# Kernel optimization log

Hardware: AMD Instinct MI355X
Metric: run time of the kernel (lower is better)

## Reference

```python
import jax, jax.numpy as jnp
import numpy as np

Q, C, D, H, K, B, T = 10000, 200, 64, 64, 4, 512, 200
MAX_DISC = 10.0


def setup_inputs() -> dict:
    key = jax.random.key(0)
    ks = jax.random.split(key, 24)

    def p(k, shape, s=0.05):
        return jax.random.normal(k, shape, jnp.float32) * s

    mid_qd = (D + C) // 2   # 132
    mid_la = (H + C) // 2   # 132
    mid_dc = (D + 1) // 2   # 32
    inp = {
        'E_q': p(ks[0], (Q + 1, D)),
        'E_c': p(ks[1], (C + 1, D)),
        'E_it': p(ks[2], (101, D)),
        'E_ut': p(ks[3], (101, D)),
        'E_nh': p(ks[4], (101, D)),
        'W_fuse': p(ks[5], (D, 3 * D)), 'b_fuse': jnp.zeros((D,), jnp.float32),
        'W_ih': p(ks[6], (3 * H, 5 * D)), 'b_ih': jnp.zeros((3 * H,), jnp.float32),
        'W_hh': p(ks[7], (3 * H, H)), 'b_hh': jnp.zeros((3 * H,), jnp.float32),
        'qd_W1': p(ks[8], (mid_qd, D)), 'qd_b1': jnp.zeros((mid_qd,), jnp.float32),
        'qd_W2': p(ks[9], (C, mid_qd)), 'qd_b2': jnp.zeros((C,), jnp.float32),
        'la_W1': p(ks[10], (mid_la, H)), 'la_b1': jnp.zeros((mid_la,), jnp.float32),
        'la_W2': p(ks[11], (C, mid_la)), 'la_b2': jnp.zeros((C,), jnp.float32),
        'dc_W1': p(ks[12], (mid_dc, D)), 'dc_b1': jnp.zeros((mid_dc,), jnp.float32),
        'dc_W2': p(ks[13], (1, mid_dc)), 'dc_b2': jnp.zeros((1,), jnp.float32),
    }
    inp['question_seq'] = jax.random.randint(ks[14], (B, T), 0, Q + 1, jnp.int32)
    inp['correct_seq'] = jax.random.randint(ks[15], (B, T), 0, 2, jnp.int32)
    inp['interval_time_seq'] = jax.random.randint(ks[16], (B, T), 0, 101, jnp.int32)
    inp['use_time_seq'] = jax.random.randint(ks[17], (B, T), 0, 101, jnp.int32)
    inp['num_hint_seq'] = jax.random.randint(ks[18], (B, T), 0, 101, jnp.int32)
    inp['num_attempt_seq'] = jax.random.randint(ks[19], (B, T), 0, 101, jnp.int32)
    # per-question concept lists + padding mask (first nc entries valid)
    q2c = jax.random.randint(ks[20], (Q + 1, K), 0, C, jnp.int32)
    nc = jax.random.randint(ks[21], (Q + 1,), 1, K + 1, jnp.int32)
    mask = (jnp.arange(K, dtype=jnp.int32)[None, :] < nc[:, None]).astype(jnp.int32)
    inp['q2c_table'] = q2c
    inp['q2c_mask'] = mask
    rows = jnp.arange(Q + 1)[:, None]
    inp['Q_table'] = jnp.zeros((Q + 1, C), jnp.float32).at[rows, q2c].max(mask.astype(jnp.float32))
    return inp


def mlp2(x, W1, b1, W2, b2):
    # MLP4Proj, num_layer=2, eval-mode dropout == identity
    return jax.nn.relu(x @ W1.T + b1) @ W2.T + b2


def gru(x, W_ih, b_ih, W_hh, b_hh):
    # torch nn.GRU, 1 layer, batch_first; gate order r,z,n
    xp = jnp.einsum('btd,gd->btg', x, W_ih) + b_ih  # [B,T,3H]

    def step(h, xp_t):
        gh = h @ W_hh.T + b_hh
        xr, xz, xn = jnp.split(xp_t, 3, axis=-1)
        hr, hz, hn = jnp.split(gh, 3, axis=-1)
        r = jax.nn.sigmoid(xr + hr)
        z = jax.nn.sigmoid(xz + hz)
        n = jnp.tanh(xn + r * hn)
        h_new = (1.0 - z) * n + z * h
        return h_new, h_new

    h0 = jnp.zeros((x.shape[0], W_hh.shape[1]), x.dtype)
    _, hs = jax.lax.scan(step, h0, jnp.swapaxes(xp, 0, 1))
    return jnp.swapaxes(hs, 0, 1)  # [B,T,H]


def reference(E_q, E_c, E_it, E_ut, E_nh, W_fuse, b_fuse, W_ih, b_ih, W_hh, b_hh,
              qd_W1, qd_b1, qd_W2, qd_b2, la_W1, la_b1, la_W2, la_b2,
              dc_W1, dc_b1, dc_W2, dc_b2, Q_table,
              question_seq, correct_seq, interval_time_seq, use_time_seq,
              num_hint_seq, num_attempt_seq, q2c_table, q2c_mask):
    qe = E_q[question_seq]                                   # [B,T,D]
    # get_concept_emb: difficulty-weighted concept fusion
    qd = jax.nn.sigmoid(mlp2(qe, qd_W1, qd_b1, qd_W2, qd_b2))  # [B,T,C]
    qc_idx = q2c_table[question_seq]                          # [B,T,K]
    msk = q2c_mask[question_seq].astype(qe.dtype)             # [B,T,K]
    rel = jnp.take_along_axis(qd, qc_idx, axis=2) * msk       # [B,T,K]
    srel = rel.sum(-1, keepdims=True) + 1e-6
    ce = (rel[..., None] * E_c[qc_idx]).sum(-2) / srel        # [B,T,D]
    corr = jnp.broadcast_to(correct_seq[..., None].astype(qe.dtype), qe.shape)
    inter = jnp.concatenate([qe, ce, corr], axis=-1)          # [B,T,3D]
    # aux-info fusion (source bug: num_attempt also uses embed_num_hint)
    ut_nh_na = jnp.concatenate([E_ut[use_time_seq], E_nh[num_hint_seq], E_nh[num_attempt_seq]], axis=-1)
    fuse = ut_nh_na @ W_fuse.T + b_fuse                       # [B,T,D]
    x = jnp.concatenate([inter, E_it[interval_time_seq], fuse], axis=-1)  # [B,T,5D]
    latent = gru(x, W_ih, b_ih, W_hh, b_hh)                   # [B,T,H]
    # predict_score on shifted slices
    lat, qe2, qs2 = latent[:, :-1], qe[:, 1:], question_seq[:, 1:]
    ua = jax.nn.sigmoid(mlp2(lat, la_W1, la_b1, la_W2, la_b2))       # [B,T-1,C]
    disc = jax.nn.sigmoid(mlp2(qe2, dc_W1, dc_b1, dc_W2, dc_b2)) * MAX_DISC  # [B,T-1,1]
    qd2 = jax.nn.sigmoid(mlp2(qe2, qd_W1, qd_b1, qd_W2, qd_b2))      # [B,T-1,C]
    Qt = Q_table[qs2]                                                # [B,T-1,C]
    ua_m = ua * Qt
    qd_m = qd2 * Qt
    sw = qd_m.sum(-1, keepdims=True) + 1e-6
    y = disc * (ua_m - qd_m) / sw
    return jax.nn.sigmoid(y.sum(-1))                                 # [B,T-1]
```

## Files before the change

kernel.cpp:

```cpp
#include <hip/hip_runtime.h>
#include <hip/hip_fp16.h>

constexpr int QN  = 10001;
constexpr int BB  = 512;
constexpr int TT  = 200;
constexpr int QPB = 32;

__device__ __forceinline__ float sigm(float x) { return 1.f / (1.f + __expf(-x)); }
__device__ __forceinline__ float tanh_fast(float x) { return 1.f - 2.f / (1.f + __expf(2.f * x)); }

__device__ __forceinline__ unsigned packh_rtne(float lo, float hi) {
    return ((unsigned)__half_as_ushort(__float2half(hi)) << 16) |
            (unsigned)__half_as_ushort(__float2half(lo));
}

typedef _Float16 half2_t __attribute__((ext_vector_type(2)));
typedef float f4v __attribute__((ext_vector_type(4)));
__device__ __forceinline__ half2_t u2h(unsigned u) {
    union { unsigned u; half2_t h; } x; x.u = u; return x.h;
}

#if __has_builtin(__builtin_amdgcn_fdot2)
__device__ __forceinline__ float fdot2u(unsigned wu, unsigned hu, float acc) {
    return __builtin_amdgcn_fdot2(u2h(wu), u2h(hu), acc, false);
}
#else
__device__ __forceinline__ float fdot2u(unsigned wu, unsigned hu, float acc) {
    float wlo = __half2float(__ushort_as_half((unsigned short)(wu & 0xffffu)));
    float whi = __half2float(__ushort_as_half((unsigned short)(wu >> 16)));
    float hlo = __half2float(__ushort_as_half((unsigned short)(hu & 0xffffu)));
    float hhi = __half2float(__ushort_as_half((unsigned short)(hu >> 16)));
    return acc + wlo * hlo + whi * hhi;
}
#endif

typedef const __attribute__((address_space(1))) void cgv_t;
typedef __attribute__((address_space(3))) void lv_t;
__device__ __forceinline__ void glds16(const float* g, float* l) {
    __builtin_amdgcn_global_load_lds((cgv_t*)g, (lv_t*)l, 16, 0, 0);
}

__global__ void k_tables(const float* __restrict__ E_c, const float* __restrict__ E_it,
                         const float* __restrict__ E_ut, const float* __restrict__ E_nh,
                         const float* __restrict__ W_fuse, const float* __restrict__ b_fuse,
                         const float* __restrict__ W_ih, const float* __restrict__ b_ih,
                         const float* __restrict__ la_W1, const float* __restrict__ la_W2,
                         float* __restrict__ T_c, float* __restrict__ T_it,
                         float* __restrict__ T_ut, float* __restrict__ T_nh, float* __restrict__ T_na,
                         float* __restrict__ bias0, float* __restrict__ Vcorr,
                         unsigned* __restrict__ w1h, unsigned* __restrict__ w2h)
{
    int blk = blockIdx.x, j = threadIdx.x;
    __shared__ float s_e[64];
    __shared__ float s_t[64];
    const int ilv4 = (j & 63) * 4 + (j >> 6);

    if (blk < 201) {
        if (j < 64) s_e[j] = E_c[blk * 64 + j];
        __syncthreads();
        float a = 0.f;
        #pragma unroll
        for (int k = 0; k < 64; k++) a += W_ih[j * 320 + 64 + k] * s_e[k];
        T_c[blk * 192 + j] = a;
    } else if (blk < 302) {
        int r = blk - 201;
        if (j < 64) s_e[j] = E_it[r * 64 + j];
        __syncthreads();
        float a = 0.f;
        #pragma unroll
        for (int k = 0; k < 64; k++) a += W_ih[j * 320 + 192 + k] * s_e[k];
        T_it[r * 256 + ilv4] = a;
    } else if (blk < 605) {
        int which = (blk - 302) / 101;
        int r     = (blk - 302) % 101;
        const float* E = (which == 0) ? E_ut : E_nh;
        int fofs = which * 64;
        if (j < 64) s_e[j] = E[r * 64 + j];
        __syncthreads();
        if (j < 64) {
            float a = 0.f;
            #pragma unroll
            for (int d = 0; d < 64; d++) a += W_fuse[j * 192 + fofs + d] * s_e[d];
            s_t[j] = a;
        }
        __syncthreads();
        float a = 0.f;
        #pragma unroll
        for (int e = 0; e < 64; e++) a += W_ih[j * 320 + 256 + e] * s_t[e];
        float* outp = (which == 0) ? T_ut : ((which == 1) ? T_nh : T_na);
        outp[r * 256 + ilv4] = a;
    } else if (blk == 605) {
        float a = b_ih[j];
        #pragma unroll
        for (int e = 0; e < 64; e++) a += W_ih[j * 320 + 256 + e] * b_fuse[e];
        bias0[j] = a;
        float v = 0.f;
        #pragma unroll
        for (int k = 0; k < 64; k++) v += W_ih[j * 320 + 128 + k];
        Vcorr[j] = v;
    } else if (blk < 628) {
        int i = (blk - 606) * 192 + j;
        int m = i >> 5, k = i & 31;
        w1h[i] = packh_rtne(la_W1[m * 64 + 2 * k], la_W1[m * 64 + 2 * k + 1]);
    } else {
        int i = (blk - 628) * 192 + j;
        if (i < 200 * 68) {
            int c = i / 68, k = i - c * 68;
            w2h[i] = (k < 66) ? packh_rtne(la_W2[c * 132 + 2 * k], la_W2[c * 132 + 2 * k + 1]) : 0u;
        }
    }
}

__global__ void __launch_bounds__(192) k_perq(
    const float* __restrict__ E_q, const float* __restrict__ W_ih,
    const float* __restrict__ qd_W1, const float* __restrict__ qd_b1,
    const float* __restrict__ qd_W2, const float* __restrict__ qd_b2,
    const float* __restrict__ dc_W1, const float* __restrict__ dc_b1,
    const float* __restrict__ dc_W2, const float* __restrict__ dc_b2,
    const int* __restrict__ q2c, const int* __restrict__ q2cm,
    const float* __restrict__ T_c,
    float* __restrict__ Xq, float* __restrict__ disc,
    float* __restrict__ qds, float* __restrict__ wdk)
{
    __shared__ float s_wbuf[192 * 66];
    __shared__ float s_qe[QPB][64];
    __shared__ float s_wq[QPB][4];
    __shared__ int   s_cq[QPB][4];
    __shared__ float s_hidw[3][136];

    const int tid = threadIdx.x, w = tid >> 6, l = tid & 63;
    const int q0 = blockIdx.x * QPB;

    for (int i = tid; i < 132 * 64; i += 192)
        s_wbuf[(i >> 6) * 66 + (i & 63)] = qd_W1[i];
    for (int i = tid; i < 32 * 64; i += 192)
        s_wbuf[(132 + (i >> 6)) * 66 + (i & 63)] = dc_W1[i];
    for (int i = tid; i < QPB * 64; i += 192) {
        int qq = i >> 6, q = q0 + qq;
        s_qe[qq][i & 63] = E_q[(q < QN ? q : 0) * 64 + (i & 63)];
    }
    __syncthreads();

    for (int qq = w; qq < QPB; qq += 3) {
        int q = q0 + qq;
        bool valid = q < QN;
        int qc = valid ? q : 0;
        int cc[4], mm[4];
        #pragma unroll
        for (int k = 0; k < 4; k++) { cc[k] = q2c[qc * 4 + k]; mm[k] = q2cm[qc * 4 + k]; }

        float qe[64];
        #pragma unroll
        for (int k4 = 0; k4 < 16; k4++) {
            float4 v = *(const float4*)(&s_qe[qq][k4 * 4]);
            qe[4 * k4] = v.x; qe[4 * k4 + 1] = v.y; qe[4 * k4 + 2] = v.z; qe[4 * k4 + 3] = v.w;
        }

        auto rowdot = [&](int r) {
            const float* wr = s_wbuf + r * 66;
            float a0 = 0.f, a1 = 0.f, a2 = 0.f, a3 = 0.f;
            #pragma unroll
            for (int jj = 0; jj < 32; jj += 4) {
                float2 w0 = *(const float2*)(wr + 2 * jj);
                float2 w1 = *(const float2*)(wr + 2 * jj + 2);
                float2 w2 = *(const float2*)(wr + 2 * jj + 4);
                float2 w3 = *(const float2*)(wr + 2 * jj + 6);
                a0 += w0.x * qe[2 * jj]     + w0.y * qe[2 * jj + 1];
                a1 += w1.x * qe[2 * jj + 2] + w1.y * qe[2 * jj + 3];
                a2 += w2.x * qe[2 * jj + 4] + w2.y * qe[2 * jj + 5];
                a3 += w3.x * qe[2 * jj + 6] + w3.y * qe[2 * jj + 7];
            }
            return (a0 + a1) + (a2 + a3);
        };

        s_hidw[w][l]      = fmaxf(rowdot(l)      + qd_b1[l],      0.f);
        s_hidw[w][64 + l] = fmaxf(rowdot(64 + l) + qd_b1[64 + l], 0.f);
        if (l < 4)
            s_hidw[w][128 + l] = fmaxf(rowdot(128 + l) + qd_b1[128 + l], 0.f);
        float dch = 0.f;
        if (l < 32) dch = fmaxf(rowdot(132 + l) + dc_b1[l], 0.f);

        int g = l >> 4, li = l & 15;
        int c = cc[g];
        float acc = 0.f;
        #pragma unroll
        for (int i = 0; i < 9; i++) {
            int m = li + 16 * i;
            if (m < 132) acc += qd_W2[c * 132 + m] * s_hidw[w][m];
        }
        acc += __shfl_xor(acc, 1); acc += __shfl_xor(acc, 2);
        acc += __shfl_xor(acc, 4); acc += __shfl_xor(acc, 8);
        float r0 = __shfl(acc, 0), r1 = __shfl(acc, 16);
        float r2 = __shfl(acc, 32), r3 = __shfl(acc, 48);

        float raw[4] = { sigm(r0 + qd_b2[cc[0]]), sigm(r1 + qd_b2[cc[1]]),
                         sigm(r2 + qd_b2[cc[2]]), sigm(r3 + qd_b2[cc[3]]) };
        float rel[4];
        #pragma unroll
        for (int k = 0; k < 4; k++) rel[k] = raw[k] * (float)mm[k];
        float sr = rel[0] + rel[1] + rel[2] + rel[3] + 1e-6f;

        float qsum = 0.f, wdv[4];
        #pragma unroll
        for (int k = 0; k < 4; k++) {
            float wd = 0.f;
            if (mm[k]) {
                bool dup = false;
                for (int jj = 0; jj < k; jj++)
                    if (mm[jj] && cc[jj] == cc[k]) dup = true;
                if (!dup) { wd = 1.f; qsum += raw[k]; }
            }
            wdv[k] = wd;
        }
        if (l < 4) { s_wq[qq][l] = rel[l] / sr; s_cq[qq][l] = cc[l]; }
        if (valid) {
            if (l < 4) wdk[q * 4 + l] = wdv[l];
            if (l == 0) qds[q] = qsum;
        }

        float dv = (l < 32) ? dch * dc_W2[l] : 0.f;
        dv += __shfl_xor(dv, 1);  dv += __shfl_xor(dv, 2);
        dv += __shfl_xor(dv, 4);  dv += __shfl_xor(dv, 8);
        dv += __shfl_xor(dv, 16);
        if (valid && l == 0) disc[q] = sigm(dv + dc_b2[0]) * 10.f;
    }

    __syncthreads();
    for (int i = tid; i < 192 * 64; i += 192) {
        int r = i >> 6, k = i & 63;
        s_wbuf[r * 66 + k] = W_ih[r * 320 + k];
    }
    __syncthreads();

    for (int qq = w; qq < QPB; qq += 3) {
        int q = q0 + qq;
        if (q >= QN) continue;

        float qe[64];
        #pragma unroll
        for (int k4 = 0; k4 < 16; k4++) {
            float4 v = *(const float4*)(&s_qe[qq][k4 * 4]);
            qe[4 * k4] = v.x; qe[4 * k4 + 1] = v.y; qe[4 * k4 + 2] = v.z; qe[4 * k4 + 3] = v.w;
        }
        float wq[4]; int cq[4];
        #pragma unroll
        for (int k = 0; k < 4; k++) { wq[k] = s_wq[qq][k]; cq[k] = s_cq[qq][k]; }

        #pragma unroll
        for (int rr = 0; rr < 3; rr++) {
            int row = rr * 64 + l;
            const float* wr = s_wbuf + row * 66;
            float a0 = 0.f, a1 = 0.f, a2 = 0.f, a3 = 0.f;
            #pragma unroll
            for (int jj = 0; jj < 32; jj += 4) {
                float2 w0 = *(const float2*)(wr + 2 * jj);
                float2 w1 = *(const float2*)(wr + 2 * jj + 2);
                float2 w2 = *(const float2*)(wr + 2 * jj + 4);
                float2 w3 = *(const float2*)(wr + 2 * jj + 6);
                a0 += w0.x * qe[2 * jj]     + w0.y * qe[2 * jj + 1];
                a1 += w1.x * qe[2 * jj + 2] + w1.y * qe[2 * jj + 3];
                a2 += w2.x * qe[2 * jj + 4] + w2.y * qe[2 * jj + 5];
                a3 += w3.x * qe[2 * jj + 6] + w3.y * qe[2 * jj + 7];
            }
            float a = (a0 + a1) + (a2 + a3);
            #pragma unroll
            for (int k = 0; k < 4; k++) a += wq[k] * T_c[cq[k] * 192 + row];
            Xq[q * 256 + l * 4 + rr] = a;
        }
    }
}

__global__ void
__launch_bounds__(256)
__attribute__((amdgpu_waves_per_eu(1, 2)))
k_gru(
    const float* __restrict__ W_hh, const float* __restrict__ b_hh,
    const float* __restrict__ XqI, const float* __restrict__ TitI, const float* __restrict__ TutI,
    const float* __restrict__ TnhI, const float* __restrict__ TnaI,
    const float* __restrict__ b0, const float* __restrict__ vc,
    const int* __restrict__ qseq, const int* __restrict__ cseq, const int* __restrict__ itseq,
    const int* __restrict__ utseq, const int* __restrict__ nhseq, const int* __restrict__ naseq,
    const unsigned* __restrict__ w1h, const float* __restrict__ la_b1,
    const unsigned* __restrict__ w2h, const float* __restrict__ la_b2,
    const int* __restrict__ q2c,
    const float* __restrict__ disc, const float* __restrict__ qds,
    const float* __restrict__ wdk, float* __restrict__ out)
{
    const int tid = threadIdx.x, b = blockIdx.x;
    const int wave = tid >> 6, j = tid & 63;
    const int j4 = 4 * j;

    __shared__ float s_gb[4][5][64][4];
    __shared__ int s_ix[6 * TT];
    __shared__ unsigned s_hp[32];
    __shared__ float s_lat[TT][66];

    const int base = b * TT;
    for (int i = tid; i < TT; i += 256) {
        s_ix[i]          = qseq[base + i];
        s_ix[TT + i]     = cseq[base + i];
        s_ix[2 * TT + i] = itseq[base + i];
        s_ix[3 * TT + i] = utseq[base + i];
        s_ix[4 * TT + i] = nhseq[base + i];
        s_ix[5 * TT + i] = naseq[base + i];
    }
    if (tid < 32) s_hp[tid] = 0u;
    __syncthreads();

    if (wave == 0) {
        unsigned wr[32], wz[32], wn[32];
        {
            const float4* p0 = (const float4*)(W_hh + j * 64);
            const float4* p1 = (const float4*)(W_hh + (64 + j) * 64);
            const float4* p2 = (const float4*)(W_hh + (128 + j) * 64);
            #pragma unroll
            for (int k = 0; k < 16; k++) {
                float4 a = p0[k], bq = p1[k], c = p2[k];
                wr[2 * k] = packh_rtne(a.x, a.y);  wr[2 * k + 1] = packh_rtne(a.z, a.w);
                wz[2 * k] = packh_rtne(bq.x, bq.y); wz[2 * k + 1] = packh_rtne(bq.z, bq.w);
                wn[2 * k] = packh_rtne(c.x, c.y);  wn[2 * k + 1] = packh_rtne(c.z, c.w);
            }
        }
        #pragma unroll
        for (int k = 0; k < 32; k++)
            asm volatile("" : "+v"(wr[k]), "+v"(wz[k]), "+v"(wn[k]));

        const float bhr = b_hh[j], bhz = b_hh[64 + j], bhn = b_hh[128 + j];
        const float b0r = b0[j],   b0z = b0[64 + j],   b0n = b0[128 + j];
        const float vcr = vc[j],   vcz = vc[64 + j],   vcn = vc[128 + j];

        float hj = 0.f;
        float cA, cB, cC, cD;

#define GISSUE(S, CCV, tt) { \
        int q_ = s_ix[tt], c_ = s_ix[TT + tt], it_ = s_ix[2 * TT + tt]; \
        int ut_ = s_ix[3 * TT + tt], nh_ = s_ix[4 * TT + tt], na_ = s_ix[5 * TT + tt]; \
        CCV = (float)c_; \
        glds16(XqI  + q_  * 256 + j4, &s_gb[S][0][0][0]); \
        glds16(TitI + it_ * 256 + j4, &s_gb[S][1][0][0]); \
        glds16(TutI + ut_ * 256 + j4, &s_gb[S][2][0][0]); \
        glds16(TnhI + nh_ * 256 + j4, &s_gb[S][3][0][0]); \
        glds16(TnaI + na_ * 256 + j4, &s_gb[S][4][0][0]); \
    }

#define STEP(S, CCV, tcur, WN, REF) { \
        asm volatile("s_waitcnt vmcnt(" WN ")" ::: "memory"); \
        f4v g0 = *(const f4v*)&s_gb[S][0][j][0]; \
        f4v g1 = *(const f4v*)&s_gb[S][1][j][0]; \
        f4v g2 = *(const f4v*)&s_gb[S][2][j][0]; \
        f4v g3 = *(const f4v*)&s_gb[S][3][j][0]; \
        f4v g4 = *(const f4v*)&s_gb[S][4][j][0]; \
        asm volatile("s_waitcnt lgkmcnt(0)" ::: "memory"); \
        float xr = b0r + CCV * vcr + (((g0.x + g1.x) + (g2.x + g3.x)) + g4.x); \
        float xz = b0z + CCV * vcz + (((g0.y + g1.y) + (g2.y + g3.y)) + g4.y); \
        float xn = b0n + CCV * vcn + (((g0.z + g1.z) + (g2.z + g3.z)) + g4.z); \
        if (REF) GISSUE(S, CCV, (tcur) + 4); \
        float ar0 = 0.f, ar1 = 0.f, ar2 = 0.f, ar3 = 0.f; \
        float az0 = 0.f, az1 = 0.f, az2 = 0.f, az3 = 0.f; \
        float an0 = 0.f, an1 = 0.f, an2 = 0.f, an3 = 0.f; \
        const uint4* hp4 = (const uint4*)s_hp; \
        _Pragma("unroll") \
        for (int k4 = 0; k4 < 8; k4++) { \
            uint4 hh = hp4[k4]; \
            ar0 = fdot2u(wr[4 * k4 + 0], hh.x, ar0); \
            ar1 = fdot2u(wr[4 * k4 + 1], hh.y, ar1); \
            ar2 = fdot2u(wr[4 * k4 + 2], hh.z, ar2); \
            ar3 = fdot2u(wr[4 * k4 + 3], hh.w, ar3); \
            az0 = fdot2u(wz[4 * k4 + 0], hh.x, az0); \
            az1 = fdot2u(wz[4 * k4 + 1], hh.y, az1); \
            az2 = fdot2u(wz[4 * k4 + 2], hh.z, az2); \
            az3 = fdot2u(wz[4 * k4 + 3], hh.w, az3); \
            an0 = fdot2u(wn[4 * k4 + 0], hh.x, an0); \
            an1 = fdot2u(wn[4 * k4 + 1], hh.y, an1); \
            an2 = fdot2u(wn[4 * k4 + 2], hh.z, an2); \
            an3 = fdot2u(wn[4 * k4 + 3], hh.w, an3); \
        } \
        float ar = ((ar0 + ar1) + (ar2 + ar3)) + bhr; \
        float az = ((az0 + az1) + (az2 + az3)) + bhz; \
        float an = ((an0 + an1) + (an2 + an3)) + bhn; \
        float r = sigm(xr + ar); \
        float z = sigm(xz + az); \
        float n = tanh_fast(xn + r * an); \
        hj = (1.f - z) * n + z * hj; \
        s_lat[tcur][j] = hj; \
        float hnb = __shfl_xor(hj, 1); \
        unsigned pk = (j & 1) ? packh_rtne(hnb, hj) : packh_rtne(hj, hnb); \
        if (!(j & 1)) s_hp[j >> 1] = pk; \
    }

        GISSUE(0, cA, 0);
        GISSUE(1, cB, 1);
        GISSUE(2, cC, 2);
        GISSUE(3, cD, 3);

        STEP(0, cA, 0, "15", 1);
        STEP(1, cB, 1, "15", 1);
        STEP(2, cC, 2, "15", 1);
        STEP(3, cD, 3, "15", 1);

        for (int t = 4; t <= TT - 8; t += 4) {
            STEP(0, cA, t,     "15", 1);
            STEP(1, cB, t + 1, "15", 1);
            STEP(2, cC, t + 2, "15", 1);
            STEP(3, cD, t + 3, "15", 1);
        }
        STEP(0, cA, TT - 4, "15", 0);
        STEP(1, cB, TT - 3, "10", 0);
        STEP(2, cC, TT - 2, "5",  0);
        STEP(3, cD, TT - 1, "0",  0);
#undef STEP
#undef GISSUE
    }
    __syncthreads();

    if (tid < TT - 1) {
        const int t = tid;
        unsigned L[32];
        {
            const float4* lp = (const float4*)&s_lat[t][0];
            #pragma unroll
            for (int kk = 0; kk < 16; kk++) {
                float4 v = lp[kk];
                L[2 * kk]     = packh_rtne(v.x, v.y);
                L[2 * kk + 1] = packh_rtne(v.z, v.w);
            }
        }

        unsigned hidpk[66];
        float hprev = 0.f;
        #pragma unroll
        for (int m = 0; m < 132; m++) {
            const unsigned* w1r = w1h + m * 32;
            float a0 = 0.f, a1 = 0.f, a2 = 0.f, a3 = 0.f;
            #pragma unroll
            for (int k = 0; k < 32; k += 4) {
                a0 = fdot2u(w1r[k],     L[k],     a0);
                a1 = fdot2u(w1r[k + 1], L[k + 1], a1);
                a2 = fdot2u(w1r[k + 2], L[k + 2], a2);
                a3 = fdot2u(w1r[k + 3], L[k + 3], a3);
            }
            float hm = fmaxf(((a0 + a1) + (a2 + a3)) + la_b1[m], 0.f);
            if (m & 1) hidpk[m >> 1] = packh_rtne(hprev, hm);
            else hprev = hm;
        }

        int q = s_ix[t + 1];
        float u[4];
        #pragma unroll
        for (int kc = 0; kc < 4; kc++) {
            int c = q2c[q * 4 + kc];
            const unsigned* w2r = w2h + c * 68;
            float u0 = 0.f, u1 = 0.f;
            #pragma unroll
            for (int k = 0; k < 66; k += 2) {
                u0 = fdot2u(w2r[k],     hidpk[k],     u0);
                u1 = fdot2u(w2r[k + 1], hidpk[k + 1], u1);
            }
            u[kc] = u0 + u1 + la_b2[c];
        }

        float us = 0.f;
        #pragma unroll
        for (int kc = 0; kc < 4; kc++) us += wdk[q * 4 + kc] * sigm(u[kc]);
        float qs = qds[q];
        float y = disc[q] * (us - qs) / (qs + 1e-6f);
        out[(size_t)b * (TT - 1) + t] = sigm(y);
    }
}

extern "C" void kernel_launch(void* const* d_in, const int* in_sizes, int n_in,
                              void* d_out, int out_size, void* d_ws, size_t ws_size,
                              hipStream_t stream)
{
    const float* E_q    = (const float*)d_in[0];
    const float* E_c    = (const float*)d_in[1];
    const float* E_it   = (const float*)d_in[2];
    const float* E_ut   = (const float*)d_in[3];
    const float* E_nh   = (const float*)d_in[4];
    const float* W_fuse = (const float*)d_in[5];
    const float* b_fuse = (const float*)d_in[6];
    const float* W_ih   = (const float*)d_in[7];
    const float* b_ih   = (const float*)d_in[8];
    const float* W_hh   = (const float*)d_in[9];
    const float* b_hh   = (const float*)d_in[10];
    const float* qd_W1  = (const float*)d_in[11];
    const float* qd_b1  = (const float*)d_in[12];
    const float* qd_W2  = (const float*)d_in[13];
    const float* qd_b2  = (const float*)d_in[14];
    const float* la_W1  = (const float*)d_in[15];
    const float* la_b1  = (const float*)d_in[16];
    const float* la_W2  = (const float*)d_in[17];
    const float* la_b2  = (const float*)d_in[18];
    const float* dc_W1  = (const float*)d_in[19];
    const float* dc_b1  = (const float*)d_in[20];
    const float* dc_W2  = (const float*)d_in[21];
    const float* dc_b2  = (const float*)d_in[22];

    int off = (in_sizes[23] == QN * 200) ? 1 : 0;
    const int* qseq  = (const int*)d_in[23 + off];
    const int* cseq  = (const int*)d_in[24 + off];
    const int* itseq = (const int*)d_in[25 + off];
    const int* utseq = (const int*)d_in[26 + off];
    const int* nhseq = (const int*)d_in[27 + off];
    const int* naseq = (const int*)d_in[28 + off];
    const int* q2c   = (const int*)d_in[29 + off];
    const int* q2cm  = (const int*)d_in[30 + off];

    float* ws = (float*)d_ws;
    size_t o = 0;
    float* T_c  = ws + o; o += (size_t)201 * 192;
    float* Tit  = ws + o; o += (size_t)101 * 256;
    float* Tut  = ws + o; o += (size_t)101 * 256;
    float* Tnh  = ws + o; o += (size_t)101 * 256;
    float* Tna  = ws + o; o += (size_t)101 * 256;
    float* b0   = ws + o; o += 192;
    float* vc   = ws + o; o += 192;
    float* Xq   = ws + o; o += (size_t)QN * 256;
    float* disc = ws + o; o += QN;
    float* qds  = ws + o; o += QN;
    float* wdk  = ws + o; o += (size_t)QN * 4;
    unsigned* w1h = (unsigned*)(ws + o); o += (size_t)132 * 32;
    unsigned* w2h = (unsigned*)(ws + o); o += (size_t)200 * 68;

    float* outp = (float*)d_out;

    k_tables<<<699, 192, 0, stream>>>(E_c, E_it, E_ut, E_nh, W_fuse, b_fuse, W_ih, b_ih,
                                      la_W1, la_W2,
                                      T_c, Tit, Tut, Tnh, Tna, b0, vc, w1h, w2h);
    k_perq<<<(QN + QPB - 1) / QPB, 192, 0, stream>>>(E_q, W_ih, qd_W1, qd_b1, qd_W2, qd_b2,
                                                     dc_W1, dc_b1, dc_W2, dc_b2, q2c, q2cm, T_c,
                                                     Xq, disc, qds, wdk);
    k_gru<<<BB, 256, 0, stream>>>(W_hh, b_hh, Xq, Tit, Tut, Tnh, Tna, b0, vc,
                                  qseq, cseq, itseq, utseq, nhseq, naseq,
                                  w1h, la_b1, w2h, la_b2, q2c, disc, qds, wdk, outp);
}
```

Baseline: 324.6 us.

## Move GRU recurrent weights to LDS and store latent as packed halves

The 96 packed-half W_hh words per lane move out of wave 0's registers into a shared-memory array filled cooperatively by all threads. The recurrent dot products now read weights from LDS every step. The latent sequence is stored as already-packed fp16 pairs, reusing the packed hidden state, so the MLP stage no longer converts it. This cuts register pressure but adds 96 LDS loads per timestep on the serial critical path, which may lengthen each step.

```diff
diff --git a/kernel.cpp b/kernel.cpp
--- a/kernel.cpp
+++ b/kernel.cpp
@@ -293,7 +293,8 @@
     __shared__ float s_gb[4][5][64][4];
     __shared__ int s_ix[6 * TT];
     __shared__ unsigned s_hp[32];
-    __shared__ float s_lat[TT][66];
+    __shared__ unsigned s_wl[96 * 64];
+    __shared__ unsigned s_lat_h[TT][33];
 
     const int base = b * TT;
     for (int i = tid; i < TT; i += 256) {
@@ -304,27 +305,16 @@
         s_ix[4 * TT + i] = nhseq[base + i];
         s_ix[5 * TT + i] = naseq[base + i];
     }
+    for (int i = tid; i < 96 * 64; i += 256) {
+        int k = i >> 6, jj = i & 63;
+        int gate = k >> 5, kk = k & 31;
+        const float* src = W_hh + (gate * 64 + jj) * 64 + 2 * kk;
+        s_wl[i] = packh_rtne(src[0], src[1]);
+    }
     if (tid < 32) s_hp[tid] = 0u;
     __syncthreads();
 
     if (wave == 0) {
-        unsigned wr[32], wz[32], wn[32];
-        {
-            const float4* p0 = (const float4*)(W_hh + j * 64);
-            const float4* p1 = (const float4*)(W_hh + (64 + j) * 64);
-            const float4* p2 = (const float4*)(W_hh + (128 + j) * 64);
-            #pragma unroll
-            for (int k = 0; k < 16; k++) {
-                float4 a = p0[k], bq = p1[k], c = p2[k];
-                wr[2 * k] = packh_rtne(a.x, a.y);  wr[2 * k + 1] = packh_rtne(a.z, a.w);
-                wz[2 * k] = packh_rtne(bq.x, bq.y); wz[2 * k + 1] = packh_rtne(bq.z, bq.w);
-                wn[2 * k] = packh_rtne(c.x, c.y);  wn[2 * k + 1] = packh_rtne(c.z, c.w);
-            }
-        }
-        #pragma unroll
-        for (int k = 0; k < 32; k++)
-            asm volatile("" : "+v"(wr[k]), "+v"(wz[k]), "+v"(wn[k]));
-
         const float bhr = b_hh[j], bhz = b_hh[64 + j], bhn = b_hh[128 + j];
         const float b0r = b0[j],   b0z = b0[64 + j],   b0n = b0[128 + j];
         const float vcr = vc[j],   vcz = vc[64 + j],   vcn = vc[128 + j];
@@ -362,18 +352,18 @@
         _Pragma("unroll") \
         for (int k4 = 0; k4 < 8; k4++) { \
             uint4 hh = hp4[k4]; \
-            ar0 = fdot2u(wr[4 * k4 + 0], hh.x, ar0); \
-            ar1 = fdot2u(wr[4 * k4 + 1], hh.y, ar1); \
-            ar2 = fdot2u(wr[4 * k4 + 2], hh.z, ar2); \
-            ar3 = fdot2u(wr[4 * k4 + 3], hh.w, ar3); \
-            az0 = fdot2u(wz[4 * k4 + 0], hh.x, az0); \
-            az1 = fdot2u(wz[4 * k4 + 1], hh.y, az1); \
-            az2 = fdot2u(wz[4 * k4 + 2], hh.z, az2); \
-            az3 = fdot2u(wz[4 * k4 + 3], hh.w, az3); \
-            an0 = fdot2u(wn[4 * k4 + 0], hh.x, an0); \
-            an1 = fdot2u(wn[4 * k4 + 1], hh.y, an1); \
-            an2 = fdot2u(wn[4 * k4 + 2], hh.z, an2); \
-            an3 = fdot2u(wn[4 * k4 + 3], hh.w, an3); \
+            ar0 = fdot2u(s_wl[(4 * k4 + 0) * 64 + j],        hh.x, ar0); \
+            ar1 = fdot2u(s_wl[(4 * k4 + 1) * 64 + j],        hh.y, ar1); \
+            ar2 = fdot2u(s_wl[(4 * k4 + 2) * 64 + j],        hh.z, ar2); \
+            ar3 = fdot2u(s_wl[(4 * k4 + 3) * 64 + j],        hh.w, ar3); \
+            az0 = fdot2u(s_wl[(32 + 4 * k4 + 0) * 64 + j],   hh.x, az0); \
+            az1 = fdot2u(s_wl[(32 + 4 * k4 + 1) * 64 + j],   hh.y, az1); \
+            az2 = fdot2u(s_wl[(32 + 4 * k4 + 2) * 64 + j],   hh.z, az2); \
+            az3 = fdot2u(s_wl[(32 + 4 * k4 + 3) * 64 + j],   hh.w, az3); \
+            an0 = fdot2u(s_wl[(64 + 4 * k4 + 0) * 64 + j],   hh.x, an0); \
+            an1 = fdot2u(s_wl[(64 + 4 * k4 + 1) * 64 + j],   hh.y, an1); \
+            an2 = fdot2u(s_wl[(64 + 4 * k4 + 2) * 64 + j],   hh.z, an2); \
+            an3 = fdot2u(s_wl[(64 + 4 * k4 + 3) * 64 + j],   hh.w, an3); \
         } \
         float ar = ((ar0 + ar1) + (ar2 + ar3)) + bhr; \
         float az = ((az0 + az1) + (az2 + az3)) + bhz; \
@@ -382,10 +372,9 @@
         float z = sigm(xz + az); \
         float n = tanh_fast(xn + r * an); \
         hj = (1.f - z) * n + z * hj; \
-        s_lat[tcur][j] = hj; \
         float hnb = __shfl_xor(hj, 1); \
         unsigned pk = (j & 1) ? packh_rtne(hnb, hj) : packh_rtne(hj, hnb); \
-        if (!(j & 1)) s_hp[j >> 1] = pk; \
+        if (!(j & 1)) { s_hp[j >> 1] = pk; s_lat_h[tcur][j >> 1] = pk; } \
     }
 
         GISSUE(0, cA, 0);
@@ -417,13 +406,8 @@
         const int t = tid;
         unsigned L[32];
         {
-            const float4* lp = (const float4*)&s_lat[t][0];
-            #pragma unroll
-            for (int kk = 0; kk < 16; kk++) {
-                float4 v = lp[kk];
-                L[2 * kk]     = packh_rtne(v.x, v.y);
-                L[2 * kk + 1] = packh_rtne(v.z, v.w);
-            }
+            #pragma unroll
+            for (int kk = 0; kk < 32; kk++) L[kk] = s_lat_h[t][kk];
         }
 
         unsigned hidpk[66];
```

Result: slower. 394.0 us (+21.4%).
